# Kernel tuning notes

Measured on AMD Instinct MI355X. Metric: run time of the kernel, lower is better.

## Reference

```python
import jax, jax.numpy as jnp
import numpy as np

N_C = 50000
N_N = 50000
E = 500000
D = 128


def _graph_conv(x_src, src, dst, n_src, n_dst, W, b):
    # DGL GraphConv, norm='both': symmetric degree normalization, then linear.
    ones = jnp.ones(src.shape, x_src.dtype)
    deg_out = jax.ops.segment_sum(ones, src, num_segments=n_src)
    deg_in = jax.ops.segment_sum(ones, dst, num_segments=n_dst)
    norm_src = jnp.maximum(deg_out, 1.0) ** -0.5  # [n_src]
    norm_dst = jnp.maximum(deg_in, 1.0) ** -0.5   # [n_dst]
    m = (x_src * norm_src[:, None])[src]          # [E, D] gather
    agg = jax.ops.segment_sum(m, dst, num_segments=n_dst)  # [n_dst, D]
    return (agg * norm_dst[:, None]) @ W + b


def _sage_conv(x_src, x_dst, src, dst, n_dst, W_self, W_neigh, b):
    # DGL SAGEConv, aggregator='mean': fc_self(h_dst) + fc_neigh(mean_neigh) + bias.
    ones = jnp.ones(src.shape, x_src.dtype)
    deg_in = jnp.maximum(jax.ops.segment_sum(ones, dst, num_segments=n_dst), 1.0)
    h_neigh = jax.ops.segment_sum(x_src[src], dst, num_segments=n_dst) / deg_in[:, None]
    return x_dst @ W_self + h_neigh @ W_neigh + b


def setup_inputs() -> dict:
    key = jax.random.key(0)
    ks = jax.random.split(key, 20)
    s = 1.0 / np.sqrt(D)
    inp = {
        'feat_C': jax.random.normal(ks[0], (N_C, D), jnp.float32),
        'feat_N': jax.random.normal(ks[1], (N_N, D), jnp.float32),
        'W1_cc': jax.random.normal(ks[2], (D, D), jnp.float32) * s,
        'b1_cc': jnp.zeros((D,), jnp.float32),
        'W1_cn': jax.random.normal(ks[3], (D, D), jnp.float32) * s,
        'b1_cn': jnp.zeros((D,), jnp.float32),
        'W1_self': jax.random.normal(ks[4], (D, D), jnp.float32) * s,
        'W1_neigh': jax.random.normal(ks[5], (D, D), jnp.float32) * s,
        'b1_nn': jnp.zeros((D,), jnp.float32),
        'W2_cc': jax.random.normal(ks[6], (D, D), jnp.float32) * s,
        'b2_cc': jnp.zeros((D,), jnp.float32),
        'W2_cn': jax.random.normal(ks[7], (D, D), jnp.float32) * s,
        'b2_cn': jnp.zeros((D,), jnp.float32),
        'W2_self': jax.random.normal(ks[8], (D, D), jnp.float32) * s,
        'W2_neigh': jax.random.normal(ks[9], (D, D), jnp.float32) * s,
        'b2_nn': jnp.zeros((D,), jnp.float32),
        'cc_src': jax.random.randint(ks[10], (E,), 0, N_C),
        'cc_dst': jax.random.randint(ks[11], (E,), 0, N_C),
        'cn_src': jax.random.randint(ks[12], (E,), 0, N_C),
        'cn_dst': jax.random.randint(ks[13], (E,), 0, N_N),
        'nn_src': jax.random.randint(ks[14], (E,), 0, N_N),
        'nn_dst': jax.random.randint(ks[15], (E,), 0, N_N),
    }
    return inp


def reference(feat_C, feat_N, W1_cc, b1_cc, W1_cn, b1_cn, W1_self, W1_neigh, b1_nn,
              W2_cc, b2_cc, W2_cn, b2_cn, W2_self, W2_neigh, b2_nn,
              cc_src, cc_dst, cn_src, cn_dst, nn_src, nn_dst):
    # layer 1 (HeteroGraphConv, aggregate='sum') + relu
    hC = _graph_conv(feat_C, cc_src, cc_dst, N_C, N_C, W1_cc, b1_cc)
    hN = (_graph_conv(feat_C, cn_src, cn_dst, N_C, N_N, W1_cn, b1_cn)
          + _sage_conv(feat_N, feat_N, nn_src, nn_dst, N_N, W1_self, W1_neigh, b1_nn))
    hC = jax.nn.relu(hC)
    hN = jax.nn.relu(hN)
    # layer 2
    oC = _graph_conv(hC, cc_src, cc_dst, N_C, N_C, W2_cc, b2_cc)
    oN = (_graph_conv(hC, cn_src, cn_dst, N_C, N_N, W2_cn, b2_cn)
          + _sage_conv(hN, hN, nn_src, nn_dst, N_N, W2_self, W2_neigh, b2_nn))
    return oC, oN
```

## Files before the change

kernel.cpp:

```cpp
#include <hip/hip_runtime.h>

#define NCN 50000
#define NE  500000
#define DF  128

#define BSHIFT 9
#define NBUCK 98
#define BK 128
#define CAP 7168
#define CHUNK 4096

typedef __attribute__((ext_vector_type(8))) short mfrag;
typedef __attribute__((ext_vector_type(4))) float facc4;

__device__ inline ushort f2bf(float x) {
    unsigned u = __float_as_uint(x);
    unsigned r = (u + 0x7FFFu + ((u >> 16) & 1u)) >> 16;
    return (ushort)r;
}
__device__ inline float bf2f(ushort h) { return __uint_as_float(((unsigned)h) << 16); }

__global__ __launch_bounds__(256) void binA_k(
    const int* __restrict__ cc_src, const int* __restrict__ cc_dst,
    const int* __restrict__ cn_src, const int* __restrict__ cn_dst,
    const int* __restrict__ nn_src, const int* __restrict__ nn_dst,
    uint2* __restrict__ R, int* __restrict__ bc)
{
    const int s = blockIdx.y;
    const int* key; const int* pay;
    switch (s) {
      case 0: key = cc_dst; pay = cc_src; break;
      case 1: key = cn_dst; pay = cn_src; break;
      case 2: key = nn_dst; pay = nn_src; break;
      case 3: key = cc_src; pay = nullptr; break;
      default: key = cn_src; pay = nullptr; break;
    }
    __shared__ uint2 rec[CHUNK];
    __shared__ int lhist[BK], lofs[BK], lcur[BK], gbase[BK];
    __shared__ int ls[256];
    const int tid = threadIdx.x;
    const int base = blockIdx.x * CHUNK;

    int k[16], p[16];
    #pragma unroll
    for (int j = 0; j < 16; ++j) {
        int e = base + j * 256 + tid;
        bool valid = (e < NE);
        k[j] = valid ? key[e] : -1;
        p[j] = (valid && pay) ? pay[e] : 0;
    }
    if (tid < BK) lhist[tid] = 0;
    __syncthreads();
    #pragma unroll
    for (int j = 0; j < 16; ++j)
        if (k[j] >= 0) atomicAdd(&lhist[k[j] >> BSHIFT], 1);
    __syncthreads();
    int v = (tid < BK) ? lhist[tid] : 0;
    ls[tid] = v;
    __syncthreads();
    #pragma unroll
    for (int off = 1; off < 128; off <<= 1) {
        int t = (tid >= off) ? ls[tid - off] : 0;
        __syncthreads();
        ls[tid] += t;
        __syncthreads();
    }
    if (tid < BK) { int e = ls[tid] - v; lofs[tid] = e; lcur[tid] = e; }
    __syncthreads();
    #pragma unroll
    for (int j = 0; j < 16; ++j) {
        if (k[j] >= 0) {
            int b = k[j] >> BSHIFT;
            int pos = atomicAdd(&lcur[b], 1);
            rec[pos] = make_uint2((unsigned)k[j], (unsigned)p[j]);
        }
    }
    __syncthreads();
    if (tid < BK) {
        int c = lcur[tid] - lofs[tid];
        gbase[tid] = (c > 0) ? atomicAdd(&bc[s * BK + tid], c) : 0;
    }
    __syncthreads();
    int total = ls[127];
    for (int i = tid; i < total; i += 256) {
        uint2 r = rec[i];
        int b = (int)(r.x >> BSHIFT);
        int gi = gbase[b] + (i - lofs[b]);
        R[((size_t)s * NBUCK + b) * CAP + gi] = r;
    }
}

__global__ __launch_bounds__(256) void binB_k(
    const uint2* __restrict__ R, const int* __restrict__ bc,
    int* __restrict__ rp3, int* __restrict__ col3, float* __restrict__ snorm2)
{
    const int b = blockIdx.x;
    const int s = blockIdx.y;
    const int tid = threadIdx.x;
    __shared__ int cnt[512];
    __shared__ int lofs[512];
    __shared__ int ls[256];
    __shared__ int sbase;

    const int nrec = bc[s * BK + b];
    const uint2* rec = R + ((size_t)s * NBUCK + b) * CAP;

    for (int i = tid; i < 512; i += 256) cnt[i] = 0;
    __syncthreads();
    for (int i = tid; i < nrec; i += 256)
        atomicAdd(&cnt[rec[i].x & 511], 1);
    __syncthreads();

    if (s >= 3) {
        float* sn = snorm2 + (size_t)(s - 3) * NCN;
        for (int j = tid; j < 512; j += 256) {
            int d = b * 512 + j;
            if (d < NCN) { int c = cnt[j]; if (c < 1) c = 1; sn[d] = rsqrtf((float)c); }
        }
        return;
    }

    {
        int v = (tid < b) ? bc[s * BK + tid] : 0;
        ls[tid] = v;
        __syncthreads();
        for (int off = 128; off > 0; off >>= 1) {
            if (tid < off) ls[tid] += ls[tid + off];
            __syncthreads();
        }
        if (tid == 0) sbase = ls[0];
        __syncthreads();
    }
    const int colBase = sbase;

    int v0 = cnt[2 * tid], v1 = cnt[2 * tid + 1];
    int pairSum = v0 + v1;
    ls[tid] = pairSum;
    __syncthreads();
    #pragma unroll
    for (int off = 1; off < 256; off <<= 1) {
        int t = (tid >= off) ? ls[tid - off] : 0;
        __syncthreads();
        ls[tid] += t;
        __syncthreads();
    }
    int excl = ls[tid] - pairSum;
    lofs[2 * tid] = excl;
    lofs[2 * tid + 1] = excl + v0;
    __syncthreads();
    const int total = ls[255];

    int* rp = rp3 + (size_t)s * (NCN + 1);
    for (int j = tid; j < 512; j += 256) {
        int d = b * 512 + j;
        if (d < NCN) rp[d] = colBase + lofs[j];
    }
    if (b == NBUCK - 1 && tid == 0) rp[NCN] = colBase + total;
    __syncthreads();

    int* col = col3 + (size_t)s * NE + colBase;
    for (int i = tid; i < nrec; i += 256) {
        uint2 r = rec[i];
        int pos = atomicAdd(&lofs[r.x & 511], 1);
        col[pos] = (int)r.y;
    }
}

__global__ __launch_bounds__(256) void wconv_k(
    const float* __restrict__ Wm0, const float* __restrict__ Wm1,
    const float* __restrict__ Wm2, const float* __restrict__ Wm3,
    const float* __restrict__ Wm4, const float* __restrict__ Wm5,
    const float* __restrict__ Wm6, const float* __restrict__ Wm7,
    ushort* __restrict__ out)
{
    const float* Ws[8] = {Wm0, Wm1, Wm2, Wm3, Wm4, Wm5, Wm6, Wm7};
    const float* W = Ws[blockIdx.x];
    ushort* o = out + (size_t)blockIdx.x * 32768;
    for (int i = threadIdx.x; i < 16384; i += 256) {
        int c = i >> 13;
        int r = i & 8191;
        int n = r >> 6;
        int jj = r & 63;
        int kk = c * 64 + (jj ^ ((n & 7) << 3));
        float wv = W[kk * 128 + n];
        ushort h = f2bf(wv);
        float lv = wv - bf2f(h);
        o[c * 16384 + r] = h;
        o[c * 16384 + 8192 + r] = f2bf(lv);
    }
}

template<int MODE>
__global__ __launch_bounds__(256) void agg_pull_k(
    const float* __restrict__ X, const int* __restrict__ rowptr,
    const int* __restrict__ colidx, const float* __restrict__ srcscale,
    float* __restrict__ out, int n)
{
    int gid = blockIdx.x * 256 + threadIdx.x;
    int row = gid >> 6;
    int lane = threadIdx.x & 63;
    if (row >= n) return;
    int e0 = rowptr[row], e1 = rowptr[row + 1];
    float ax = 0.f, ay = 0.f;
    int e = e0;
    for (; e + 4 <= e1; e += 4) {
        int s0 = colidx[e], s1 = colidx[e + 1], s2 = colidx[e + 2], s3 = colidx[e + 3];
        float c0 = srcscale ? srcscale[s0] : 1.0f;
        float c1 = srcscale ? srcscale[s1] : 1.0f;
        float c2 = srcscale ? srcscale[s2] : 1.0f;
        float c3 = srcscale ? srcscale[s3] : 1.0f;
        const float2 u0 = *(const float2*)(X + (size_t)s0 * DF + lane * 2);
        const float2 u1 = *(const float2*)(X + (size_t)s1 * DF + lane * 2);
        const float2 u2 = *(const float2*)(X + (size_t)s2 * DF + lane * 2);
        const float2 u3 = *(const float2*)(X + (size_t)s3 * DF + lane * 2);
        ax = fmaf(u0.x, c0, ax); ay = fmaf(u0.y, c0, ay);
        ax = fmaf(u1.x, c1, ax); ay = fmaf(u1.y, c1, ay);
        ax = fmaf(u2.x, c2, ax); ay = fmaf(u2.y, c2, ay);
        ax = fmaf(u3.x, c3, ax); ay = fmaf(u3.y, c3, ay);
    }
    for (; e < e1; ++e) {
        int s0 = colidx[e];
        float c0 = srcscale ? srcscale[s0] : 1.0f;
        const float2 u0 = *(const float2*)(X + (size_t)s0 * DF + lane * 2);
        ax = fmaf(u0.x, c0, ax); ay = fmaf(u0.y, c0, ay);
    }
    int deg = e1 - e0; if (deg < 1) deg = 1;
    float dsc = (MODE == 0) ? rsqrtf((float)deg) : (1.0f / (float)deg);
    float2 o; o.x = ax * dsc; o.y = ay * dsc;
    *(float2*)(out + (size_t)row * DF + lane * 2) = o;
}

template<int NSRC, bool RELU>
__global__ __launch_bounds__(256, 2) void mgemm_k(
    const float* __restrict__ A0, const float* __restrict__ A1, const float* __restrict__ A2,
    const ushort* __restrict__ Wi0, const ushort* __restrict__ Wi1, const ushort* __restrict__ Wi2,
    const float* __restrict__ b0, const float* __restrict__ b1,
    float* __restrict__ Y, int M)
{
    constexpr int NCH = 2 * NSRC;
    __shared__ ushort Asm[16384];
    __shared__ ushort Wsm[16384];
    const int tid = threadIdx.x;
    const int l = tid & 63;
    const int wv = tid >> 6;
    const int r0 = blockIdx.x * 128;

    const float*  Aarr[3] = {A0, A1, A2};
    const ushort* Warr[3] = {Wi0, Wi1, Wi2};

    const int srow = tid >> 1;
    const int shalf = tid & 1;
    int grow = r0 + srow; if (grow > M - 1) grow = M - 1;

    facc4 acc[2][8];
    #pragma unroll
    for (int rt = 0; rt < 2; ++rt)
        #pragma unroll
        for (int ct = 0; ct < 8; ++ct)
            acc[rt][ct] = (facc4){0.f, 0.f, 0.f, 0.f};

    float4 ArA[8], ArB[8];
    uint4  Wr[8];

    auto loadA = [&](int c, float4* ar) {
        int s = c >> 1, k0 = (c & 1) * 64;
        const float4* ap = (const float4*)(Aarr[s] + (size_t)grow * DF + k0 + shalf * 32);
        #pragma unroll
        for (int i = 0; i < 8; ++i) ar[i] = ap[i];
    };
    auto loadW = [&](int c) {
        int s = c >> 1, cl = c & 1;
        const uint4* wp = (const uint4*)(Warr[s] + cl * 16384);
        #pragma unroll
        for (int i = 0; i < 8; ++i) Wr[i] = wp[i * 256 + tid];
    };
    auto writeW = [&]() {
        uint4* wd = (uint4*)Wsm;
        #pragma unroll
        for (int i = 0; i < 8; ++i) wd[i * 256 + tid] = Wr[i];
    };
    auto writeA = [&](const float4* ar) {
        #pragma unroll
        for (int g = 0; g < 4; ++g) {
            uint hp[4], lp[4];
            #pragma unroll
            for (int q = 0; q < 2; ++q) {
                float4 vq = ar[g * 2 + q];
                ushort h0 = f2bf(vq.x); ushort l0 = f2bf(vq.x - bf2f(h0));
                ushort h1 = f2bf(vq.y); ushort l1 = f2bf(vq.y - bf2f(h1));
                ushort h2 = f2bf(vq.z); ushort l2 = f2bf(vq.z - bf2f(h2));
                ushort h3 = f2bf(vq.w); ushort l3 = f2bf(vq.w - bf2f(h3));
                hp[q * 2]     = (uint)h0 | ((uint)h1 << 16);
                hp[q * 2 + 1] = (uint)h2 | ((uint)h3 << 16);
                lp[q * 2]     = (uint)l0 | ((uint)l1 << 16);
                lp[q * 2 + 1] = (uint)l2 | ((uint)l3 << 16);
            }
            int kbyte = shalf * 64 + g * 16;
            int idx = srow * 64 + ((kbyte ^ ((srow & 7) << 4)) >> 1);
            *(uint4*)(Asm + idx)        = make_uint4(hp[0], hp[1], hp[2], hp[3]);
            *(uint4*)(Asm + 8192 + idx) = make_uint4(lp[0], lp[1], lp[2], lp[3]);
        }
    };

    loadA(0, ArA);
    loadW(0);

    #pragma unroll
    for (int c = 0; c < NCH; ++c) {
        __syncthreads();
        if (c & 1) writeA(ArB); else writeA(ArA);
        writeW();
        if (c + 1 < NCH) {
            if (c & 1) loadA(c + 1, ArA); else loadA(c + 1, ArB);
            loadW(c + 1);
        }
        __syncthreads();
        #pragma unroll
        for (int ks = 0; ks < 2; ++ks) {
            const int kbyte = ks * 64 + (l >> 4) * 16;
            mfrag a_hi[2], a_lo[2];
            #pragma unroll
            for (int rt = 0; rt < 2; ++rt) {
                int row = wv * 32 + rt * 16 + (l & 15);
                int idx = row * 64 + ((kbyte ^ ((row & 7) << 4)) >> 1);
                a_hi[rt] = *(const mfrag*)(Asm + idx);
                a_lo[rt] = *(const mfrag*)(Asm + 8192 + idx);
            }
            #pragma unroll
            for (int ct = 0; ct < 8; ++ct) {
                int col = ct * 16 + (l & 15);
                int widx = col * 64 + ((kbyte ^ ((col & 7) << 4)) >> 1);
                mfrag w_hi = *(const mfrag*)(Wsm + widx);
                mfrag w_lo = *(const mfrag*)(Wsm + 8192 + widx);
                #pragma unroll
                for (int rt = 0; rt < 2; ++rt) {
                    acc[rt][ct] = __builtin_amdgcn_mfma_f32_16x16x32_bf16(a_hi[rt], w_hi, acc[rt][ct], 0, 0, 0);
                    acc[rt][ct] = __builtin_amdgcn_mfma_f32_16x16x32_bf16(a_hi[rt], w_lo, acc[rt][ct], 0, 0, 0);
                    acc[rt][ct] = __builtin_amdgcn_mfma_f32_16x16x32_bf16(a_lo[rt], w_hi, acc[rt][ct], 0, 0, 0);
                }
            }
        }
    }

    float bias[8];
    #pragma unroll
    for (int ct = 0; ct < 8; ++ct) {
        int col = ct * 16 + (l & 15);
        float bv = b0 ? b0[col] : 0.f;
        if (b1) bv += b1[col];
        bias[ct] = bv;
    }
    #pragma unroll
    for (int rt = 0; rt < 2; ++rt) {
        #pragma unroll
        for (int q = 0; q < 4; ++q) {
            int row = r0 + wv * 32 + rt * 16 + (l >> 4) * 4 + q;
            if (row < M) {
                #pragma unroll
                for (int ct = 0; ct < 8; ++ct) {
                    float v = acc[rt][ct][q] + bias[ct];
                    if (RELU) v = fmaxf(v, 0.f);
                    Y[(size_t)row * DF + ct * 16 + (l & 15)] = v;
                }
            }
        }
    }
}

extern "C" void kernel_launch(void* const* d_in, const int* in_sizes, int n_in,
                              void* d_out, int out_size, void* d_ws, size_t ws_size,
                              hipStream_t stream)
{
    (void)in_sizes; (void)n_in; (void)out_size; (void)ws_size;
    const float* feat_C   = (const float*)d_in[0];
    const float* feat_N   = (const float*)d_in[1];
    const float* W1_cc    = (const float*)d_in[2];
    const float* b1_cc    = (const float*)d_in[3];
    const float* W1_cn    = (const float*)d_in[4];
    const float* b1_cn    = (const float*)d_in[5];
    const float* W1_self  = (const float*)d_in[6];
    const float* W1_neigh = (const float*)d_in[7];
    const float* b1_nn    = (const float*)d_in[8];
    const float* W2_cc    = (const float*)d_in[9];
    const float* b2_cc    = (const float*)d_in[10];
    const float* W2_cn    = (const float*)d_in[11];
    const float* b2_cn    = (const float*)d_in[12];
    const float* W2_self  = (const float*)d_in[13];
    const float* W2_neigh = (const float*)d_in[14];
    const float* b2_nn    = (const float*)d_in[15];
    const int* cc_src = (const int*)d_in[16];
    const int* cc_dst = (const int*)d_in[17];
    const int* cn_src = (const int*)d_in[18];
    const int* cn_dst = (const int*)d_in[19];
    const int* nn_src = (const int*)d_in[20];
    const int* nn_dst = (const int*)d_in[21];

    char* ws = (char*)d_ws;
    size_t off = 0;
    auto take = [&](size_t bytes) -> char* {
        char* p = ws + off;
        off = (off + bytes + 255) & ~(size_t)255;
        return p;
    };
    int*    rp3    = (int*)take((size_t)3 * (NCN + 1) * sizeof(int));
    int*    col3   = (int*)take((size_t)3 * NE * sizeof(int));
    float*  snorm2 = (float*)take((size_t)2 * NCN * sizeof(float));
    int*    bc     = (int*)take((size_t)5 * BK * sizeof(int));
    ushort* Wimg   = (ushort*)take((size_t)8 * 32768 * sizeof(ushort));
    char* bigRegion = take((size_t)2 * NCN * DF * sizeof(float));
    uint2* R    = (uint2*)bigRegion;
    float* aggA = (float*)bigRegion;
    float* aggB = (float*)(bigRegion + (size_t)NCN * DF * sizeof(float));

    float* oC = (float*)d_out;
    float* oN = oC + (size_t)NCN * DF;

    const int binABlocks = (NE + CHUNK - 1) / CHUNK;
    const int aggBlocks  = (NCN * 64 + 255) / 256;
    const int gemmBlocks = (NCN + 127) / 128;

    const ushort* I0 = Wimg;
    auto img = [&](int m) { return I0 + (size_t)m * 32768; };

    hipMemsetAsync(bc, 0, (size_t)5 * BK * sizeof(int), stream);
    binA_k<<<dim3(binABlocks, 5), 256, 0, stream>>>(cc_src, cc_dst, cn_src, cn_dst,
                                                    nn_src, nn_dst, R, bc);
    binB_k<<<dim3(NBUCK, 5), 256, 0, stream>>>(R, bc, rp3, col3, snorm2);
    wconv_k<<<8, 256, 0, stream>>>(W1_cc, W1_cn, W1_neigh, W1_self,
                                   W2_cc, W2_cn, W2_neigh, W2_self, Wimg);

    agg_pull_k<0><<<aggBlocks, 256, 0, stream>>>(feat_C, rp3 + 0 * (NCN + 1), col3 + 0 * NE,
                                                 snorm2 + 0 * NCN, aggA, NCN);
    mgemm_k<1, true><<<gemmBlocks, 256, 0, stream>>>(aggA, nullptr, nullptr,
                                                     img(0), nullptr, nullptr,
                                                     b1_cc, nullptr, oC, NCN);
    agg_pull_k<0><<<aggBlocks, 256, 0, stream>>>(feat_C, rp3 + 1 * (NCN + 1), col3 + 1 * NE,
                                                 snorm2 + 1 * NCN, aggA, NCN);
    agg_pull_k<1><<<aggBlocks, 256, 0, stream>>>(feat_N, rp3 + 2 * (NCN + 1), col3 + 2 * NE,
                                                 nullptr, aggB, NCN);
    mgemm_k<3, true><<<gemmBlocks, 256, 0, stream>>>(aggA, aggB, feat_N,
                                                     img(1), img(2), img(3),
                                                     b1_cn, b1_nn, oN, NCN);

    agg_pull_k<0><<<aggBlocks, 256, 0, stream>>>(oC, rp3 + 0 * (NCN + 1), col3 + 0 * NE,
                                                 snorm2 + 0 * NCN, aggA, NCN);
    agg_pull_k<0><<<aggBlocks, 256, 0, stream>>>(oC, rp3 + 1 * (NCN + 1), col3 + 1 * NE,
                                                 snorm2 + 1 * NCN, aggB, NCN);
    mgemm_k<1, false><<<gemmBlocks, 256, 0, stream>>>(aggA, nullptr, nullptr,
                                                      img(4), nullptr, nullptr,
                                                      b2_cc, nullptr, oC, NCN);
    agg_pull_k<1><<<aggBlocks, 256, 0, stream>>>(oN, rp3 + 2 * (NCN + 1), col3 + 2 * NE,
                                                 nullptr, aggA, NCN);
    mgemm_k<3, false><<<gemmBlocks, 256, 0, stream>>>(aggB, aggA, oN,
                                                      img(5), img(6), img(7),
                                                      b2_cn, b2_nn, oN, NCN);
}
```

Before: 428.5 us.

## Emit pre-split bf16 aggregates and load GEMM A fragments directly from global

The aggregation kernels now write hi/lo bf16 split images instead of fp32 rows, and the two GraphConv aggregations sharing a source are merged into one launch over a 2D grid. The GEMM drops its A shared-memory stage and loads MFMA fragments straight from global, converting fp32 only for the self-feature source. Occupancy rises to 3 blocks per CU since shared memory use is halved. This cuts intermediate traffic and the A staging cost, in exchange for uncoalesced per-lane global fragment loads in the GEMM.

```diff
diff --git a/kernel.cpp b/kernel.cpp
--- a/kernel.cpp
+++ b/kernel.cpp
@@ -19,6 +19,16 @@
     return (ushort)r;
 }
 __device__ inline float bf2f(ushort h) { return __uint_as_float(((unsigned)h) << 16); }
+
+__device__ inline void store_split(ushort* __restrict__ T, int row, int lane,
+                                   float vx, float vy) {
+    ushort hx = f2bf(vx); ushort lx = f2bf(vx - bf2f(hx));
+    ushort hy = f2bf(vy); ushort ly = f2bf(vy - bf2f(hy));
+    uint hp = (uint)hx | ((uint)hy << 16);
+    uint lp = (uint)lx | ((uint)ly << 16);
+    *(uint*)(T + (size_t)row * DF + lane * 2) = hp;
+    *(uint*)(T + (size_t)NCN * DF + (size_t)row * DF + lane * 2) = lp;
+}
 
 __global__ __launch_bounds__(256) void binA_k(
     const int* __restrict__ cc_src, const int* __restrict__ cc_dst,
@@ -190,25 +200,26 @@
     }
 }
 
-template<int MODE>
-__global__ __launch_bounds__(256) void agg_pull_k(
-    const float* __restrict__ X, const int* __restrict__ rowptr,
-    const int* __restrict__ colidx, const float* __restrict__ srcscale,
-    float* __restrict__ out, int n)
-{
+__global__ __launch_bounds__(256) void agg2_k(
+    const float* __restrict__ X,
+    const int* __restrict__ rpA, const int* __restrict__ colA,
+    const float* __restrict__ scA, ushort* __restrict__ outA,
+    const int* __restrict__ rpB, const int* __restrict__ colB,
+    const float* __restrict__ scB, ushort* __restrict__ outB)
+{
+    const int* rp; const int* col; const float* sc; ushort* out;
+    if (blockIdx.y == 0) { rp = rpA; col = colA; sc = scA; out = outA; }
+    else                 { rp = rpB; col = colB; sc = scB; out = outB; }
     int gid = blockIdx.x * 256 + threadIdx.x;
     int row = gid >> 6;
     int lane = threadIdx.x & 63;
-    if (row >= n) return;
-    int e0 = rowptr[row], e1 = rowptr[row + 1];
+    if (row >= NCN) return;
+    int e0 = rp[row], e1 = rp[row + 1];
     float ax = 0.f, ay = 0.f;
     int e = e0;
     for (; e + 4 <= e1; e += 4) {
-        int s0 = colidx[e], s1 = colidx[e + 1], s2 = colidx[e + 2], s3 = colidx[e + 3];
-        float c0 = srcscale ? srcscale[s0] : 1.0f;
-        float c1 = srcscale ? srcscale[s1] : 1.0f;
-        float c2 = srcscale ? srcscale[s2] : 1.0f;
-        float c3 = srcscale ? srcscale[s3] : 1.0f;
+        int s0 = col[e], s1 = col[e + 1], s2 = col[e + 2], s3 = col[e + 3];
+        float c0 = sc[s0], c1 = sc[s1], c2 = sc[s2], c3 = sc[s3];
         const float2 u0 = *(const float2*)(X + (size_t)s0 * DF + lane * 2);
         const float2 u1 = *(const float2*)(X + (size_t)s1 * DF + lane * 2);
         const float2 u2 = *(const float2*)(X + (size_t)s2 * DF + lane * 2);
@@ -219,38 +230,70 @@
         ax = fmaf(u3.x, c3, ax); ay = fmaf(u3.y, c3, ay);
     }
     for (; e < e1; ++e) {
-        int s0 = colidx[e];
-        float c0 = srcscale ? srcscale[s0] : 1.0f;
+        int s0 = col[e];
+        float c0 = sc[s0];
         const float2 u0 = *(const float2*)(X + (size_t)s0 * DF + lane * 2);
         ax = fmaf(u0.x, c0, ax); ay = fmaf(u0.y, c0, ay);
     }
     int deg = e1 - e0; if (deg < 1) deg = 1;
-    float dsc = (MODE == 0) ? rsqrtf((float)deg) : (1.0f / (float)deg);
-    float2 o; o.x = ax * dsc; o.y = ay * dsc;
-    *(float2*)(out + (size_t)row * DF + lane * 2) = o;
-}
-
-template<int NSRC, bool RELU>
-__global__ __launch_bounds__(256, 2) void mgemm_k(
-    const float* __restrict__ A0, const float* __restrict__ A1, const float* __restrict__ A2,
+    float dsc = rsqrtf((float)deg);
+    store_split(out, row, lane, ax * dsc, ay * dsc);
+}
+
+__global__ __launch_bounds__(256) void agg1_k(
+    const float* __restrict__ X, const int* __restrict__ rp,
+    const int* __restrict__ col, ushort* __restrict__ out)
+{
+    int gid = blockIdx.x * 256 + threadIdx.x;
+    int row = gid >> 6;
+    int lane = threadIdx.x & 63;
+    if (row >= NCN) return;
+    int e0 = rp[row], e1 = rp[row + 1];
+    float ax = 0.f, ay = 0.f;
+    int e = e0;
+    for (; e + 4 <= e1; e += 4) {
+        int s0 = col[e], s1 = col[e + 1], s2 = col[e + 2], s3 = col[e + 3];
+        const float2 u0 = *(const float2*)(X + (size_t)s0 * DF + lane * 2);
+        const float2 u1 = *(const float2*)(X + (size_t)s1 * DF + lane * 2);
+        const float2 u2 = *(const float2*)(X + (size_t)s2 * DF + lane * 2);
+        const float2 u3 = *(const float2*)(X + (size_t)s3 * DF + lane * 2);
+        ax += u0.x + u1.x + u2.x + u3.x;
+        ay += u0.y + u1.y + u2.y + u3.y;
+    }
+    for (; e < e1; ++e) {
+        int s0 = col[e];
+        const float2 u0 = *(const float2*)(X + (size_t)s0 * DF + lane * 2);
+        ax += u0.x; ay += u0.y;
+    }
+    int deg = e1 - e0; if (deg < 1) deg = 1;
+    float dsc = 1.0f / (float)deg;
+    store_split(out, row, lane, ax * dsc, ay * dsc);
+}
+
+template<int NSRC, bool RELU, int F32S>
+__global__ __launch_bounds__(256, 3) void mgemm_k(
+    const void* __restrict__ A0, const void* __restrict__ A1, const void* __restrict__ A2,
     const ushort* __restrict__ Wi0, const ushort* __restrict__ Wi1, const ushort* __restrict__ Wi2,
     const float* __restrict__ b0, const float* __restrict__ b1,
     float* __restrict__ Y, int M)
 {
     constexpr int NCH = 2 * NSRC;
-    __shared__ ushort Asm[16384];
     __shared__ ushort Wsm[16384];
     const int tid = threadIdx.x;
     const int l = tid & 63;
     const int wv = tid >> 6;
     const int r0 = blockIdx.x * 128;
 
-    const float*  Aarr[3] = {A0, A1, A2};
+    const void*   Aarr[3] = {A0, A1, A2};
     const ushort* Warr[3] = {Wi0, Wi1, Wi2};
 
-    const int srow = tid >> 1;
-    const int shalf = tid & 1;
-    int grow = r0 + srow; if (grow > M - 1) grow = M - 1;
+    int arow[2];
+    #pragma unroll
+    for (int rt = 0; rt < 2; ++rt) {
+        int r = r0 + wv * 32 + rt * 16 + (l & 15);
+        arow[rt] = (r < M) ? r : (M - 1);
+    }
+    const int kgrp = (l >> 4) * 8;
 
     facc4 acc[2][8];
     #pragma unroll
@@ -259,84 +302,81 @@
         for (int ct = 0; ct < 8; ++ct)
             acc[rt][ct] = (facc4){0.f, 0.f, 0.f, 0.f};
 
-    float4 ArA[8], ArB[8];
-    uint4  Wr[8];
-
-    auto loadA = [&](int c, float4* ar) {
-        int s = c >> 1, k0 = (c & 1) * 64;
-        const float4* ap = (const float4*)(Aarr[s] + (size_t)grow * DF + k0 + shalf * 32);
-        #pragma unroll
-        for (int i = 0; i < 8; ++i) ar[i] = ap[i];
-    };
-    auto loadW = [&](int c) {
-        int s = c >> 1, cl = c & 1;
-        const uint4* wp = (const uint4*)(Warr[s] + cl * 16384);
+    uint4 Wr[8];
+    auto loadWr = [&](int c) {
+        int s = c >> 1, half = c & 1;
+        const uint4* wp = (const uint4*)(Warr[s] + half * 16384);
         #pragma unroll
         for (int i = 0; i < 8; ++i) Wr[i] = wp[i * 256 + tid];
     };
-    auto writeW = [&]() {
-        uint4* wd = (uint4*)Wsm;
-        #pragma unroll
-        for (int i = 0; i < 8; ++i) wd[i * 256 + tid] = Wr[i];
+
+    mfrag ah[2][2], al[2][2];
+    auto loadA = [&](int c) {
+        int s = c >> 1;
+        int k0 = (c & 1) * 64;
+        if (s == F32S) {
+            const float* F = (const float*)Aarr[s];
+            #pragma unroll
+            for (int ks = 0; ks < 2; ++ks)
+                #pragma unroll
+                for (int rt = 0; rt < 2; ++rt) {
+                    const float* p = F + (size_t)arow[rt] * DF + k0 + ks * 32 + kgrp;
+                    float4 v0 = *(const float4*)p;
+                    float4 v1 = *(const float4*)(p + 4);
+                    union { mfrag m; ushort u[8]; } H, L;
+                    float vv0[4] = {v0.x, v0.y, v0.z, v0.w};
+                    float vv1[4] = {v1.x, v1.y, v1.z, v1.w};
+                    #pragma unroll
+                    for (int j = 0; j < 4; ++j) {
+                        ushort h = f2bf(vv0[j]);
+                        H.u[j] = h; L.u[j] = f2bf(vv0[j] - bf2f(h));
+                    }
+                    #pragma unroll
+                    for (int j = 0; j < 4; ++j) {
+                        ushort h = f2bf(vv1[j]);
+                        H.u[4 + j] = h; L.u[4 + j] = f2bf(vv1[j] - bf2f(h));
+                    }
+                    ah[ks][rt] = H.m; al[ks][rt] = L.m;
+                }
+        } else {
+            const ushort* T = (const ushort*)Aarr[s];
+            #pragma unroll
+            for (int ks = 0; ks < 2; ++ks)
+                #pragma unroll
+                for (int rt = 0; rt < 2; ++rt) {
+                    size_t o = (size_t)arow[rt] * DF + k0 + ks * 32 + kgrp;
+                    ah[ks][rt] = *(const mfrag*)(T + o);
+                    al[ks][rt] = *(const mfrag*)(T + (size_t)NCN * DF + o);
+                }
+        }
     };
-    auto writeA = [&](const float4* ar) {
-        #pragma unroll
-        for (int g = 0; g < 4; ++g) {
-            uint hp[4], lp[4];
+
+    loadWr(0);
+    #pragma unroll
+    for (int c = 0; c < NCH; ++c) {
+        __syncthreads();
+        {
+            uint4* wd = (uint4*)Wsm;
             #pragma unroll
-            for (int q = 0; q < 2; ++q) {
-                float4 vq = ar[g * 2 + q];
-                ushort h0 = f2bf(vq.x); ushort l0 = f2bf(vq.x - bf2f(h0));
-                ushort h1 = f2bf(vq.y); ushort l1 = f2bf(vq.y - bf2f(h1));
-                ushort h2 = f2bf(vq.z); ushort l2 = f2bf(vq.z - bf2f(h2));
-                ushort h3 = f2bf(vq.w); ushort l3 = f2bf(vq.w - bf2f(h3));
-                hp[q * 2]     = (uint)h0 | ((uint)h1 << 16);
-                hp[q * 2 + 1] = (uint)h2 | ((uint)h3 << 16);
-                lp[q * 2]     = (uint)l0 | ((uint)l1 << 16);
-                lp[q * 2 + 1] = (uint)l2 | ((uint)l3 << 16);
-            }
-            int kbyte = shalf * 64 + g * 16;
-            int idx = srow * 64 + ((kbyte ^ ((srow & 7) << 4)) >> 1);
-            *(uint4*)(Asm + idx)        = make_uint4(hp[0], hp[1], hp[2], hp[3]);
-            *(uint4*)(Asm + 8192 + idx) = make_uint4(lp[0], lp[1], lp[2], lp[3]);
-        }
-    };
-
-    loadA(0, ArA);
-    loadW(0);
-
-    #pragma unroll
-    for (int c = 0; c < NCH; ++c) {
-        __syncthreads();
-        if (c & 1) writeA(ArB); else writeA(ArA);
-        writeW();
-        if (c + 1 < NCH) {
-            if (c & 1) loadA(c + 1, ArA); else loadA(c + 1, ArB);
-            loadW(c + 1);
-        }
+            for (int i = 0; i < 8; ++i) wd[i * 256 + tid] = Wr[i];
+        }
+        loadA(c);
+        if (c + 1 < NCH) loadWr(c + 1);
         __syncthreads();
         #pragma unroll
         for (int ks = 0; ks < 2; ++ks) {
             const int kbyte = ks * 64 + (l >> 4) * 16;
-            mfrag a_hi[2], a_lo[2];
-            #pragma unroll
-            for (int rt = 0; rt < 2; ++rt) {
-                int row = wv * 32 + rt * 16 + (l & 15);
-                int idx = row * 64 + ((kbyte ^ ((row & 7) << 4)) >> 1);
-                a_hi[rt] = *(const mfrag*)(Asm + idx);
-                a_lo[rt] = *(const mfrag*)(Asm + 8192 + idx);
-            }
             #pragma unroll
             for (int ct = 0; ct < 8; ++ct) {
-                int col = ct * 16 + (l & 15);
-                int widx = col * 64 + ((kbyte ^ ((col & 7) << 4)) >> 1);
+                int colc = ct * 16 + (l & 15);
+                int widx = colc * 64 + ((kbyte ^ ((colc & 7) << 4)) >> 1);
                 mfrag w_hi = *(const mfrag*)(Wsm + widx);
                 mfrag w_lo = *(const mfrag*)(Wsm + 8192 + widx);
                 #pragma unroll
                 for (int rt = 0; rt < 2; ++rt) {
-                    acc[rt][ct] = __builtin_amdgcn_mfma_f32_16x16x32_bf16(a_hi[rt], w_hi, acc[rt][ct], 0, 0, 0);
-                    acc[rt][ct] = __builtin_amdgcn_mfma_f32_16x16x32_bf16(a_hi[rt], w_lo, acc[rt][ct], 0, 0, 0);
-                    acc[rt][ct] = __builtin_amdgcn_mfma_f32_16x16x32_bf16(a_lo[rt], w_hi, acc[rt][ct], 0, 0, 0);
+                    acc[rt][ct] = __builtin_amdgcn_mfma_f32_16x16x32_bf16(ah[ks][rt], w_hi, acc[rt][ct], 0, 0, 0);
+                    acc[rt][ct] = __builtin_amdgcn_mfma_f32_16x16x32_bf16(ah[ks][rt], w_lo, acc[rt][ct], 0, 0, 0);
+                    acc[rt][ct] = __builtin_amdgcn_mfma_f32_16x16x32_bf16(al[ks][rt], w_hi, acc[rt][ct], 0, 0, 0);
                 }
             }
         }
@@ -345,9 +385,9 @@
     float bias[8];
     #pragma unroll
     for (int ct = 0; ct < 8; ++ct) {
-        int col = ct * 16 + (l & 15);
-        float bv = b0 ? b0[col] : 0.f;
-        if (b1) bv += b1[col];
+        int colc = ct * 16 + (l & 15);
+        float bv = b0 ? b0[colc] : 0.f;
+        if (b1) bv += b1[colc];
         bias[ct] = bv;
     }
     #pragma unroll
@@ -407,10 +447,10 @@
     float*  snorm2 = (float*)take((size_t)2 * NCN * sizeof(float));
     int*    bc     = (int*)take((size_t)5 * BK * sizeof(int));
     ushort* Wimg   = (ushort*)take((size_t)8 * 32768 * sizeof(ushort));
-    char* bigRegion = take((size_t)2 * NCN * DF * sizeof(float));
-    uint2* R    = (uint2*)bigRegion;
-    float* aggA = (float*)bigRegion;
-    float* aggB = (float*)(bigRegion + (size_t)NCN * DF * sizeof(float));
+    char* bigRegion = take((size_t)2 * 2 * NCN * DF * sizeof(ushort));
+    uint2*  R  = (uint2*)bigRegion;
+    ushort* P0 = (ushort*)bigRegion;
+    ushort* P1 = (ushort*)(bigRegion + (size_t)2 * NCN * DF * sizeof(ushort));
 
     float* oC = (float*)d_out;
     float* oN = oC + (size_t)NCN * DF;
@@ -419,8 +459,15 @@
     const int aggBlocks  = (NCN * 64 + 255) / 256;
     const int gemmBlocks = (NCN + 127) / 128;
 
-    const ushort* I0 = Wimg;
-    auto img = [&](int m) { return I0 + (size_t)m * 32768; };
+    auto img = [&](int m) { return (const ushort*)(Wimg + (size_t)m * 32768); };
+    const int* rpCC = rp3 + 0 * (NCN + 1);
+    const int* rpCN = rp3 + 1 * (NCN + 1);
+    const int* rpNN = rp3 + 2 * (NCN + 1);
+    const int* colCC = col3 + 0 * NE;
+    const int* colCN = col3 + 1 * NE;
+    const int* colNN = col3 + 2 * NE;
+    const float* snCC = snorm2 + 0 * NCN;
+    const float* snCN = snorm2 + 1 * NCN;
 
     hipMemsetAsync(bc, 0, (size_t)5 * BK * sizeof(int), stream);
     binA_k<<<dim3(binABlocks, 5), 256, 0, stream>>>(cc_src, cc_dst, cn_src, cn_dst,
@@ -429,29 +476,25 @@
     wconv_k<<<8, 256, 0, stream>>>(W1_cc, W1_cn, W1_neigh, W1_self,
                                    W2_cc, W2_cn, W2_neigh, W2_self, Wimg);
 
-    agg_pull_k<0><<<aggBlocks, 256, 0, stream>>>(feat_C, rp3 + 0 * (NCN + 1), col3 + 0 * NE,
-                                                 snorm2 + 0 * NCN, aggA, NCN);
-    mgemm_k<1, true><<<gemmBlocks, 256, 0, stream>>>(aggA, nullptr, nullptr,
-                                                     img(0), nullptr, nullptr,
-                                                     b1_cc, nullptr, oC, NCN);
-    agg_pull_k<0><<<aggBlocks, 256, 0, stream>>>(feat_C, rp3 + 1 * (NCN + 1), col3 + 1 * NE,
-                                                 snorm2 + 1 * NCN, aggA, NCN);
-    agg_pull_k<1><<<aggBlocks, 256, 0, stream>>>(feat_N, rp3 + 2 * (NCN + 1), col3 + 2 * NE,
-                                                 nullptr, aggB, NCN);
-    mgemm_k<3, true><<<gemmBlocks, 256, 0, stream>>>(aggA, aggB, feat_N,
-                                                     img(1), img(2), img(3),
-                                                     b1_cn, b1_nn, oN, NCN);
-
-    agg_pull_k<0><<<aggBlocks, 256, 0, stream>>>(oC, rp3 + 0 * (NCN + 1), col3 + 0 * NE,
-                                                 snorm2 + 0 * NCN, aggA, NCN);
-    agg_pull_k<0><<<aggBlocks, 256, 0, stream>>>(oC, rp3 + 1 * (NCN + 1), col3 + 1 * NE,
-                                                 snorm2 + 1 * NCN, aggB, NCN);
-    mgemm_k<1, false><<<gemmBlocks, 256, 0, stream>>>(aggA, nullptr, nullptr,
-                                                      img(4), nullptr, nullptr,
-                                                      b2_cc, nullptr, oC, NCN);
-    agg_pull_k<1><<<aggBlocks, 256, 0, stream>>>(oN, rp3 + 2 * (NCN + 1), col3 + 2 * NE,
-                                                 nullptr, aggA, NCN);
-    mgemm_k<3, false><<<gemmBlocks, 256, 0, stream>>>(aggB, aggA, oN,
-                                                      img(5), img(6), img(7),
-                                                      b2_cn, b2_nn, oN, NCN);
-}
+    agg2_k<<<dim3(aggBlocks, 2), 256, 0, stream>>>(feat_C,
+                                                   rpCC, colCC, snCC, P0,
+                                                   rpCN, colCN, snCN, P1);
+    mgemm_k<1, true, -1><<<gemmBlocks, 256, 0, stream>>>(P0, nullptr, nullptr,
+                                                         img(0), nullptr, nullptr,
+                                                         b1_cc, nullptr, oC, NCN);
+    agg1_k<<<aggBlocks, 256, 0, stream>>>(feat_N, rpNN, colNN, P0);
+    mgemm_k<3, true, 2><<<gemmBlocks, 256, 0, stream>>>(P1, P0, feat_N,
+                                                        img(1), img(2), img(3),
+                                                        b1_cn, b1_nn, oN, NCN);
+
+    agg2_k<<<dim3(aggBlocks, 2), 256, 0, stream>>>(oC,
+                                                   rpCN, colCN, snCN, P1,
+                                                   rpCC, colCC, snCC, P0);
+    mgemm_k<1, false, -1><<<gemmBlocks, 256, 0, stream>>>(P0, nullptr, nullptr,
+                                                          img(4), nullptr, nullptr,
+                                                          b2_cc, nullptr, oC, NCN);
+    agg1_k<<<aggBlocks, 256, 0, stream>>>(oN, rpNN, colNN, P0);
+    mgemm_k<3, false, 2><<<gemmBlocks, 256, 0, stream>>>(P1, P0, oN,
+                                                         img(5), img(6), img(7),
+                                                         b2_cn, b2_nn, oN, NCN);
+}
```

Measured after the change: 416.4 us. 2.8% less time.
